# Kernel tuning notes

Hardware: AMD Instinct MI355X
Metric: run time of the kernel (lower is better)

The kernel has to match this reference:

```python
import jax, jax.numpy as jnp
from jax import lax
import numpy as np

DIM = 768        # d_model (mamba-130m)
D_IN = 1024      # vision encoder feature dim
NQ = 384         # num_queries
NB = 12          # num_blocks
BATCH = 2
LSEQ = 1024      # image tokens
DI = 2 * DIM     # mamba d_inner (expand=2)
DS = 16          # d_state
DC = 4           # d_conv
DTR = 48         # dt_rank = ceil(768/16)
NH = 16          # attention heads
HD = DIM // NH
NM = NB + 2      # mamba instances: fwd-enc, bwd-enc, one per block


def _ln(x, g, b):
    m = jnp.mean(x, -1, keepdims=True)
    v = jnp.mean((x - m) ** 2, -1, keepdims=True)
    return (x - m) * lax.rsqrt(v + 1e-5) * g + b


def _mamba(x, in_w, conv_w, conv_b, xproj_w, dt_w, dt_b, A_log, Dp, out_w):
    # x: (B, L, DIM)
    Bb = x.shape[0]
    xz = x @ in_w.T                      # (B, L, 2*DI)
    xi, z = jnp.split(xz, 2, -1)
    # depthwise causal conv1d over time
    xc = lax.conv_general_dilated(xi.transpose(0, 2, 1), conv_w[:, None, :], (1,),
                                  [(DC - 1, 0)], feature_group_count=DI,
                                  dimension_numbers=('NCH', 'OIH', 'NCH'))
    xc = jax.nn.silu((xc + conv_b[None, :, None]).transpose(0, 2, 1))  # (B, L, DI)
    dbl = xc @ xproj_w.T                 # (B, L, DTR + 2*DS)
    dt, Bm, Cm = jnp.split(dbl, [DTR, DTR + DS], -1)
    dt = jax.nn.softplus(dt @ dt_w.T + dt_b)   # (B, L, DI)
    A = -jnp.exp(A_log)                        # (DI, DS)
    dA = jnp.exp(dt[..., None] * A)            # (B, L, DI, DS)
    dBx = dt[..., None] * Bm[:, :, None, :] * xc[..., None]

    def step(h, inp):
        dA_t, dBx_t, C_t = inp
        h = dA_t * h + dBx_t
        return h, jnp.einsum('bds,bs->bd', h, C_t)

    h0 = jnp.zeros((Bb, DI, DS), x.dtype)
    _, ys = lax.scan(step, h0, (dA.transpose(1, 0, 2, 3), dBx.transpose(1, 0, 2, 3), Cm.transpose(1, 0, 2)))
    y = ys.transpose(1, 0, 2) + Dp * xc
    y = y * jax.nn.silu(z)
    return y @ out_w.T


def _local_allowed(nq, nk):
    # matches Attention.get_local_mask: query i attends to its contiguous key block
    kpq, extra = nk // nq, nk % nq
    i = jnp.arange(nq)
    start = i * kpq + jnp.minimum(i, extra)
    end = start + kpq + (i < extra)
    k = jnp.arange(nk)
    return (k[None, :] >= start[:, None]) & (k[None, :] < end[:, None])


def _mha(q_in, kv, in_w, in_b, out_w, out_b, allowed):
    # nn.MultiheadAttention(dim, 16, batch_first=True) cross-attention
    wq, wk, wv = jnp.split(in_w, 3, 0)
    bq, bk, bv = jnp.split(in_b, 3, 0)
    Bb = q_in.shape[0]
    q = (q_in @ wq.T + bq).reshape(Bb, -1, NH, HD)
    k = (kv @ wk.T + bk).reshape(Bb, -1, NH, HD)
    v = (kv @ wv.T + bv).reshape(Bb, -1, NH, HD)
    s = jnp.einsum('bqhd,bkhd->bhqk', q, k) / np.float32(np.sqrt(HD))
    s = jnp.where(allowed[None, None], s, -jnp.inf)
    a = jax.nn.softmax(s, -1)
    o = jnp.einsum('bhqk,bkhd->bqhd', a, v).reshape(Bb, -1, DIM)
    return o @ out_w.T + out_b


def _model(img_emb, queries, vision_proj_w, vision_proj_b, ln_vision_g, ln_vision_b,
           mamba_in_w, mamba_conv_w, mamba_conv_b, mamba_xproj_w, mamba_dt_w, mamba_dt_b,
           mamba_A_log, mamba_D, mamba_out_w, seq_norm_g, seq_norm_b,
           attn_in_w, attn_in_b, attn_out_w, attn_out_b, cross_w, cross_b):
    mp = lambda i: (mamba_in_w[i], mamba_conv_w[i], mamba_conv_b[i], mamba_xproj_w[i],
                    mamba_dt_w[i], mamba_dt_b[i], mamba_A_log[i], mamba_D[i], mamba_out_w[i])
    feats = _ln(img_emb @ vision_proj_w.T + vision_proj_b, ln_vision_g, ln_vision_b)
    fwd = _mamba(feats, *mp(0))
    bwd = jnp.flip(_mamba(jnp.flip(feats, 1), *mp(1)), 1)
    c = fwd + bwd + feats
    x = jnp.broadcast_to(queries, (img_emb.shape[0], NQ, DIM))
    allowed = _local_allowed(NQ, c.shape[1])
    for l in range(NB):
        x = _ln(x, seq_norm_g[l], seq_norm_b[l])
        x = _mamba(x, *mp(l + 2)) + x
        score = _mha(x, c, attn_in_w[l], attn_in_b[l], attn_out_w[l], attn_out_b[l], allowed)
        x = jnp.concatenate([x, score], -1) @ cross_w[l].T + cross_b[l]
    return x


_model_jit = jax.jit(_model)


def setup_inputs() -> dict:
    key = jax.random.key(0)
    ks = iter(jax.random.split(key, 24))
    rn = lambda shape, s=0.02: jax.random.normal(next(ks), shape, jnp.float32) * s
    A_log = jnp.broadcast_to(jnp.log(jnp.arange(1, DS + 1, dtype=jnp.float32)), (NM, DI, DS))
    return {
        'img_emb': rn((BATCH, LSEQ, D_IN), 1.0),
        'queries': rn((1, NQ, DIM)),
        'vision_proj_w': rn((DIM, D_IN)),
        'vision_proj_b': jnp.zeros((DIM,), jnp.float32),
        'ln_vision_g': jnp.ones((DIM,), jnp.float32),
        'ln_vision_b': jnp.zeros((DIM,), jnp.float32),
        'mamba_in_w': rn((NM, 2 * DI, DIM)),
        'mamba_conv_w': rn((NM, DI, DC), 0.1),
        'mamba_conv_b': jnp.zeros((NM, DI), jnp.float32),
        'mamba_xproj_w': rn((NM, DTR + 2 * DS, DI)),
        'mamba_dt_w': rn((NM, DI, DTR), 0.1),
        'mamba_dt_b': rn((NM, DI), 0.5),
        'mamba_A_log': A_log,
        'mamba_D': jnp.ones((NM, DI), jnp.float32),
        'mamba_out_w': rn((NM, DIM, DI)),
        'seq_norm_g': jnp.ones((NB, DIM), jnp.float32),
        'seq_norm_b': jnp.zeros((NB, DIM), jnp.float32),
        'attn_in_w': rn((NB, 3 * DIM, DIM)),
        'attn_in_b': jnp.zeros((NB, 3 * DIM), jnp.float32),
        'attn_out_w': rn((NB, DIM, DIM)),
        'attn_out_b': jnp.zeros((NB, DIM), jnp.float32),
        'cross_w': rn((NB, DIM, 2 * DIM)),
        'cross_b': jnp.zeros((NB, DIM), jnp.float32),
    }


def reference(img_emb, queries, vision_proj_w, vision_proj_b, ln_vision_g, ln_vision_b,
              mamba_in_w, mamba_conv_w, mamba_conv_b, mamba_xproj_w, mamba_dt_w, mamba_dt_b,
              mamba_A_log, mamba_D, mamba_out_w, seq_norm_g, seq_norm_b,
              attn_in_w, attn_in_b, attn_out_w, attn_out_b, cross_w, cross_b):
    return _model_jit(img_emb, queries, vision_proj_w, vision_proj_b, ln_vision_g, ln_vision_b,
                      mamba_in_w, mamba_conv_w, mamba_conv_b, mamba_xproj_w, mamba_dt_w, mamba_dt_b,
                      mamba_A_log, mamba_D, mamba_out_w, seq_norm_g, seq_norm_b,
                      attn_in_w, attn_in_b, attn_out_w, attn_out_b, cross_w, cross_b)
```

## Files before the change

kernel.cpp:

```cpp
#include <hip/hip_runtime.h>
#include <hip/hip_bf16.h>

#define DIMQ 768
#define D_IN 1024
#define NQ 384
#define NBK 12
#define BATCH 2
#define LSEQ 1024
#define DI 1536
#define DS 16
#define DTR 48
#define NH 16
#define HD 48

typedef __attribute__((ext_vector_type(8))) short short8;
typedef __attribute__((ext_vector_type(4))) float f32x4;

#define GF_BIAS 1
#define GF_SOFTPLUS 2
#define EPI_BIAS 1
#define EPI_ADDT 2

#define LOG2E 1.4426950408889634f

__device__ __forceinline__ unsigned short f2bf(float f) {
    unsigned int u = __builtin_bit_cast(unsigned int, f);
    u = (u + 0x7FFFu + ((u >> 16) & 1u)) >> 16;
    return (unsigned short)u;
}
__device__ __forceinline__ float bf2f(unsigned short h) {
    unsigned int u = ((unsigned int)h) << 16;
    return __builtin_bit_cast(float, u);
}

__device__ __forceinline__ void gload_lds16(const void* g, void* l) {
    __builtin_amdgcn_global_load_lds(
        (const __attribute__((address_space(1))) void*)g,
        (__attribute__((address_space(3))) void*)l, 16, 0, 0);
}

struct WTab {
    const float* src[10];
    long long dstOff[10];
    long long ps[10];
    int cum[10];
    int rows[10], cols[10], dcols[10];
    int n;
    int total;
};

__global__ void wconv_kernel(unsigned short* __restrict__ dst, WTab T)
{
    const int i = blockIdx.x * 256 + threadIdx.x;
    if (i >= T.total) return;
    int sI = 0;
    while (i >= T.cum[sI]) ++sI;
    const int e = i - (sI ? T.cum[sI - 1] : 0);
    const int dcols = T.dcols[sI];
    const int r = e / dcols;
    const int c = e - r * dcols;
    float v = 0.f;
    if (r < T.rows[sI] && c < T.cols[sI]) v = T.src[sI][(long long)r * T.cols[sI] + c];
    const unsigned short h = f2bf(v);
    const unsigned short l = f2bf(v - bf2f(h));
    dst[T.dstOff[sI] + e] = h;
    dst[T.dstOff[sI] + T.ps[sI] + e] = l;
}

__global__ __launch_bounds__(256, 4)
void gemm_direct(const float* __restrict__ Ag, const unsigned short* __restrict__ Bhl,
                 float* __restrict__ Cg, const float* __restrict__ biasg,
                 int M, int N, int K, int lda, int ldb, int ldc,
                 long long sA, long long sB, long long sC, long long sBias,
                 long long planeB, int flags)
{
    __shared__ __align__(16) unsigned short As[2][64][40];
    __shared__ __align__(16) unsigned short Bs[2][128][32];

    const int z = blockIdx.z;
    const float* A = Ag + (size_t)z * sA;
    const unsigned short* Bhi = Bhl + (size_t)z * sB;
    const unsigned short* Blo = Bhi + planeB;
    float* C = Cg + (size_t)z * sC;

    const int mBase = blockIdx.x * 64;
    const int nBase = blockIdx.y * 128;
    const int tid = threadIdx.x, lane = tid & 63, wave = tid >> 6;
    const int lm = lane & 15, lq = lane >> 4;
    const int wn = wave * 32;
    const int arow = tid >> 2, aq = tid & 3;
    const int brow = lane >> 2;
    const int bcol = (lane & 3) * 8;

    f32x4 acc[4][2] = {};
    const int ktiles = (K + 31) >> 5;

    for (int t = 0; t < ktiles; ++t) {
        const int kb = t * 32;
#pragma unroll
        for (int cc = 0; cc < 4; ++cc) {
            const int chunk = wave * 4 + cc;
            const int pl = chunk >> 3;
            const int r16 = chunk & 7;
            const unsigned short* bp = pl ? Blo : Bhi;
            const int n = nBase + r16 * 16 + brow;
            const unsigned short* g = bp + (size_t)n * ldb + kb + bcol;
            gload_lds16(g, &Bs[pl][r16 * 16][0]);
        }
        {
            const int gr = mBase + arow;
            const int col = kb + aq * 8;
            const float* src = A + (size_t)gr * lda + col;
            float v[8];
#pragma unroll
            for (int u = 0; u < 2; ++u) {
                float4 t4 = make_float4(0.f, 0.f, 0.f, 0.f);
                if (col + u * 4 < K) t4 = *(const float4*)(src + u * 4);
                v[u*4+0]=t4.x; v[u*4+1]=t4.y; v[u*4+2]=t4.z; v[u*4+3]=t4.w;
            }
            short8 ph, plv;
#pragma unroll
            for (int j = 0; j < 8; ++j) {
                unsigned short h = f2bf(v[j]);
                ph[j] = (short)h;
                plv[j] = (short)f2bf(v[j] - bf2f(h));
            }
            *(short8*)&As[0][arow][aq * 8] = ph;
            *(short8*)&As[1][arow][aq * 8] = plv;
        }
        __syncthreads();
        short8 ah[4], al[4], bh[2], bl[2];
#pragma unroll
        for (int i = 0; i < 4; ++i) {
            ah[i] = *(const short8*)&As[0][16*i + lm][lq * 8];
            al[i] = *(const short8*)&As[1][16*i + lm][lq * 8];
        }
#pragma unroll
        for (int j = 0; j < 2; ++j) {
            bh[j] = *(const short8*)&Bs[0][wn + 16*j + lm][lq * 8];
            bl[j] = *(const short8*)&Bs[1][wn + 16*j + lm][lq * 8];
        }
#pragma unroll
        for (int i = 0; i < 4; ++i)
#pragma unroll
            for (int j = 0; j < 2; ++j) {
                acc[i][j] = __builtin_amdgcn_mfma_f32_16x16x32_bf16(ah[i], bh[j], acc[i][j], 0, 0, 0);
                acc[i][j] = __builtin_amdgcn_mfma_f32_16x16x32_bf16(ah[i], bl[j], acc[i][j], 0, 0, 0);
                acc[i][j] = __builtin_amdgcn_mfma_f32_16x16x32_bf16(al[i], bh[j], acc[i][j], 0, 0, 0);
            }
        __syncthreads();
    }

#pragma unroll
    for (int i = 0; i < 4; ++i)
#pragma unroll
        for (int j = 0; j < 2; ++j)
#pragma unroll
            for (int r = 0; r < 4; ++r) {
                const int m = mBase + i*16 + lq*4 + r;
                const int n = nBase + wn + j*16 + lm;
                float v = acc[i][j][r];
                if (flags & GF_BIAS)     v += biasg[(size_t)z * sBias + n];
                if (flags & GF_SOFTPLUS) v = (v > 20.f) ? v : log1pf(expf(v));
                C[(size_t)m * ldc + n] = v;
            }
}

__global__ __launch_bounds__(256, 4)
void gemm_splitk(const float* __restrict__ Ag, const unsigned short* __restrict__ Bhl,
                 float* __restrict__ Cp,
                 int M, int kLen, int S, int lda, int ldb, int ldP,
                 long long sA, long long sB, long long planeB)
{
    __shared__ __align__(16) unsigned short As[2][64][40];
    __shared__ __align__(16) unsigned short Bs[2][128][32];

    const int bz = blockIdx.z;
    const int s = bz % S, z = bz / S;
    const int kOff = s * kLen;
    const float* A = Ag + (size_t)z * sA;
    const unsigned short* Bhi = Bhl + (size_t)z * sB;
    const unsigned short* Blo = Bhi + planeB;

    const int mBase = blockIdx.x * 64;
    const int nBase = blockIdx.y * 128;
    const int tid = threadIdx.x, lane = tid & 63, wave = tid >> 6;
    const int lm = lane & 15, lq = lane >> 4;
    const int wn = wave * 32;
    const int arow = tid >> 2, aq = tid & 3;
    const int brow = lane >> 2;
    const int bcol = (lane & 3) * 8;

    f32x4 acc[4][2] = {};
    const int ktiles = kLen >> 5;

    for (int t = 0; t < ktiles; ++t) {
        const int kb = kOff + t * 32;
#pragma unroll
        for (int cc = 0; cc < 4; ++cc) {
            const int chunk = wave * 4 + cc;
            const int pl = chunk >> 3;
            const int r16 = chunk & 7;
            const unsigned short* bp = pl ? Blo : Bhi;
            const int n = nBase + r16 * 16 + brow;
            gload_lds16(bp + (size_t)n * ldb + kb + bcol, &Bs[pl][r16 * 16][0]);
        }
        {
            const int gr = mBase + arow;
            const float* src = A + (size_t)gr * lda + kb + aq * 8;
            float v[8];
#pragma unroll
            for (int u = 0; u < 2; ++u) {
                const float4 t4 = *(const float4*)(src + u * 4);
                v[u*4+0]=t4.x; v[u*4+1]=t4.y; v[u*4+2]=t4.z; v[u*4+3]=t4.w;
            }
            short8 ph, plv;
#pragma unroll
            for (int j = 0; j < 8; ++j) {
                unsigned short h = f2bf(v[j]);
                ph[j] = (short)h;
                plv[j] = (short)f2bf(v[j] - bf2f(h));
            }
            *(short8*)&As[0][arow][aq * 8] = ph;
            *(short8*)&As[1][arow][aq * 8] = plv;
        }
        __syncthreads();
        short8 ah[4], al[4], bh[2], bl[2];
#pragma unroll
        for (int i = 0; i < 4; ++i) {
            ah[i] = *(const short8*)&As[0][16*i + lm][lq * 8];
            al[i] = *(const short8*)&As[1][16*i + lm][lq * 8];
        }
#pragma unroll
        for (int j = 0; j < 2; ++j) {
            bh[j] = *(const short8*)&Bs[0][wn + 16*j + lm][lq * 8];
            bl[j] = *(const short8*)&Bs[1][wn + 16*j + lm][lq * 8];
        }
#pragma unroll
        for (int i = 0; i < 4; ++i)
#pragma unroll
            for (int j = 0; j < 2; ++j) {
                acc[i][j] = __builtin_amdgcn_mfma_f32_16x16x32_bf16(ah[i], bh[j], acc[i][j], 0, 0, 0);
                acc[i][j] = __builtin_amdgcn_mfma_f32_16x16x32_bf16(ah[i], bl[j], acc[i][j], 0, 0, 0);
                acc[i][j] = __builtin_amdgcn_mfma_f32_16x16x32_bf16(al[i], bh[j], acc[i][j], 0, 0, 0);
            }
        __syncthreads();
    }

    float* Cb = Cp + (size_t)bz * M * ldP;
#pragma unroll
    for (int i = 0; i < 4; ++i)
#pragma unroll
        for (int j = 0; j < 2; ++j)
#pragma unroll
            for (int r = 0; r < 4; ++r) {
                const int m = mBase + i*16 + lq*4 + r;
                const int n = nBase + wn + j*16 + lm;
                Cb[(size_t)m * ldP + n] = acc[i][j][r];
            }
}

__global__ void epi_kernel(const float* __restrict__ Cp, float* __restrict__ outF,
                           const float* __restrict__ bias, const float* __restrict__ addT,
                           int Z, int S, int M, int N, int ldP, int ldOut,
                           long long sOutZ, long long sBiasZ, int ldAdd, int flags)
{
    const int n4 = N >> 2;
    const int idx = blockIdx.x * 256 + threadIdx.x;
    if (idx >= Z * M * n4) return;
    const int c4 = idx % n4;
    const int rem = idx / n4;
    const int m = rem % M;
    const int z = rem / M;
    const int n = c4 * 4;
    const float* base = Cp + ((size_t)z * S * M + m) * ldP + n;
    float4 v = *(const float4*)base;
    for (int s = 1; s < S; ++s) {
        const float4 u = *(const float4*)(base + (size_t)s * M * ldP);
        v.x += u.x; v.y += u.y; v.z += u.z; v.w += u.w;
    }
    if (flags & EPI_BIAS) {
        const float4 b4 = *(const float4*)(bias + (size_t)z * sBiasZ + n);
        v.x += b4.x; v.y += b4.y; v.z += b4.z; v.w += b4.w;
    }
    if (flags & EPI_ADDT) {
        const float4 a4 = *(const float4*)(addT + (size_t)m * ldAdd + n);
        v.x += a4.x; v.y += a4.y; v.z += a4.z; v.w += a4.w;
    }
    *(float4*)(outF + (size_t)z * sOutZ + (size_t)m * ldOut + n) = v;
}

__global__ void ln_kernel(const float* __restrict__ in, float* __restrict__ out,
                          const float* __restrict__ g, const float* __restrict__ b, int rows)
{
    const int row = blockIdx.x * 4 + (threadIdx.x >> 6);
    const int lane = threadIdx.x & 63;
    if (row >= rows) return;
    const float* p = in + (size_t)row * DIMQ;
    float v[12], s = 0.f, s2 = 0.f;
#pragma unroll
    for (int j = 0; j < 12; ++j) {
        v[j] = p[j*64 + lane];
        s += v[j];
        s2 += v[j]*v[j];
    }
#pragma unroll
    for (int o = 32; o; o >>= 1) { s += __shfl_xor(s, o); s2 += __shfl_xor(s2, o); }
    const float mean = s * (1.f/768.f);
    const float var  = s2 * (1.f/768.f) - mean*mean;
    const float inv  = rsqrtf(var + 1e-5f);
    float* q = out + (size_t)row * DIMQ;
#pragma unroll
    for (int j = 0; j < 12; ++j) {
        const int c = j*64 + lane;
        q[c] = (v[j] - mean) * inv * g[c] + b[c];
    }
}

__global__ void conv_kernel(const float* __restrict__ xz, float* __restrict__ xc,
                            const float* __restrict__ cw, const float* __restrict__ cb,
                            int Bn, int L, int instShift)
{
    const int idx = blockIdx.x * 256 + threadIdx.x;
    const int total = Bn * L * (DI/4);
    if (idx >= total) return;
    const int d4 = idx % (DI/4);
    const int t  = (idx / (DI/4)) % L;
    const int b  = idx / (L * (DI/4));
    const int inst = b >> instShift;
    const int d = d4 * 4;
    const float* base = xz + (size_t)(b * L) * 3072 + d;
    const float4 w0 = *(const float4*)(cw + (size_t)(inst*DI + d + 0) * 4);
    const float4 w1 = *(const float4*)(cw + (size_t)(inst*DI + d + 1) * 4);
    const float4 w2 = *(const float4*)(cw + (size_t)(inst*DI + d + 2) * 4);
    const float4 w3 = *(const float4*)(cw + (size_t)(inst*DI + d + 3) * 4);
    float4 acc = *(const float4*)(cb + (size_t)inst*DI + d);
    float4 xv[4];
#pragma unroll
    for (int j = 0; j < 4; ++j) {
        const int tt = t - 3 + j;
        xv[j] = (tt >= 0) ? *(const float4*)(base + (size_t)tt * 3072) : make_float4(0,0,0,0);
    }
    acc.x += xv[0].x*w0.x + xv[1].x*w0.y + xv[2].x*w0.z + xv[3].x*w0.w;
    acc.y += xv[0].y*w1.x + xv[1].y*w1.y + xv[2].y*w1.z + xv[3].y*w1.w;
    acc.z += xv[0].z*w2.x + xv[1].z*w2.y + xv[2].z*w2.z + xv[3].z*w2.w;
    acc.w += xv[0].w*w3.x + xv[1].w*w3.y + xv[2].w*w3.z + xv[3].w*w3.w;
    float4 o;
    o.x = acc.x / (1.f + expf(-acc.x));
    o.y = acc.y / (1.f + expf(-acc.y));
    o.z = acc.z / (1.f + expf(-acc.z));
    o.w = acc.w / (1.f + expf(-acc.w));
    *(float4*)(xc + (size_t)(b * L + t) * DI + d) = o;
}

__global__ __launch_bounds__(256)
void scan_p1(const float* __restrict__ dt, const float* __restrict__ dbl,
             const float* __restrict__ xc, const float* __restrict__ A_log,
             float* __restrict__ hend, float* __restrict__ sumdt,
             int L, int CL, int Bn, int instShift)
{
    const int d = blockIdx.x * 256 + threadIdx.x;
    const int b = blockIdx.y;
    const int c = blockIdx.z;
    const int inst = b >> instShift;
    const float* ap = A_log + ((size_t)inst * DI + d) * DS;
    float A2[16];
#pragma unroll
    for (int s = 0; s < 16; ++s) A2[s] = -expf(ap[s]) * LOG2E;
    float h[16] = {};
    float sd = 0.f;
    const int t0 = c * CL;
    const size_t rowbase = (size_t)b * L;
    for (int t = t0; t < t0 + CL; ++t) {
        const size_t row = rowbase + t;
        const float dtv = dt[row * DI + d];
        const float xcv = xc[row * DI + d];
        float Bv[16];
        *(float4*)(Bv + 0)  = *(const float4*)(dbl + row * 80 + 48);
        *(float4*)(Bv + 4)  = *(const float4*)(dbl + row * 80 + 52);
        *(float4*)(Bv + 8)  = *(const float4*)(dbl + row * 80 + 56);
        *(float4*)(Bv + 12) = *(const float4*)(dbl + row * 80 + 60);
        sd += dtv;
        const float bx = dtv * xcv;
#pragma unroll
        for (int s = 0; s < 16; ++s)
            h[s] = exp2f(dtv * A2[s]) * h[s] + bx * Bv[s];
    }
    float* hp = hend + (((size_t)c * Bn + b) * DI + d) * DS;
#pragma unroll
    for (int s = 0; s < 16; s += 4)
        *(float4*)(hp + s) = make_float4(h[s], h[s+1], h[s+2], h[s+3]);
    sumdt[((size_t)c * Bn + b) * DI + d] = sd;
}

__global__ void scan_p2(const float* __restrict__ hend, const float* __restrict__ sumdt,
                        const float* __restrict__ A_log, float* __restrict__ hstart,
                        int NC, int Bn, int instShift)
{
    const int gid = blockIdx.x * 256 + threadIdx.x;
    const int s = gid & 15;
    const int rem = gid >> 4;
    const int d = rem % DI;
    const int b = rem / DI;
    const int inst = b >> instShift;
    const float A2 = -expf(A_log[((size_t)inst * DI + d) * DS + s]) * LOG2E;
    float carry = 0.f;
    for (int c = 0; c < NC; ++c) {
        const size_t off = (((size_t)c * Bn + b) * DI + d) * DS + s;
        hstart[off] = carry;
        carry = exp2f(A2 * sumdt[((size_t)c * Bn + b) * DI + d]) * carry + hend[off];
    }
}

__global__ __launch_bounds__(256)
void scan_p3(const float* __restrict__ dt, const float* __restrict__ dbl,
             const float* __restrict__ xc, const float* __restrict__ xz,
             const float* __restrict__ A_log, const float* __restrict__ Dp,
             const float* __restrict__ hstart, float* __restrict__ y,
             int L, int CL, int Bn, int instShift)
{
    const int d = blockIdx.x * 256 + threadIdx.x;
    const int b = blockIdx.y;
    const int c = blockIdx.z;
    const int inst = b >> instShift;
    const float* ap = A_log + ((size_t)inst * DI + d) * DS;
    float A2[16];
#pragma unroll
    for (int s = 0; s < 16; ++s) A2[s] = -expf(ap[s]) * LOG2E;
    const float Dd = Dp[(size_t)inst * DI + d];
    float h[16];
    const float* hp = hstart + (((size_t)c * Bn + b) * DI + d) * DS;
#pragma unroll
    for (int s = 0; s < 16; s += 4) {
        const float4 t4 = *(const float4*)(hp + s);
        h[s] = t4.x; h[s+1] = t4.y; h[s+2] = t4.z; h[s+3] = t4.w;
    }
    const int t0 = c * CL;
    const size_t rowbase = (size_t)b * L;
    for (int t = t0; t < t0 + CL; ++t) {
        const size_t row = rowbase + t;
        const float dtv = dt[row * DI + d];
        const float xcv = xc[row * DI + d];
        const float zv  = xz[row * 3072 + DI + d];
        float Bv[16], Cv[16];
        *(float4*)(Bv + 0)  = *(const float4*)(dbl + row * 80 + 48);
        *(float4*)(Bv + 4)  = *(const float4*)(dbl + row * 80 + 52);
        *(float4*)(Bv + 8)  = *(const float4*)(dbl + row * 80 + 56);
        *(float4*)(Bv + 12) = *(const float4*)(dbl + row * 80 + 60);
        *(float4*)(Cv + 0)  = *(const float4*)(dbl + row * 80 + 64);
        *(float4*)(Cv + 4)  = *(const float4*)(dbl + row * 80 + 68);
        *(float4*)(Cv + 8)  = *(const float4*)(dbl + row * 80 + 72);
        *(float4*)(Cv + 12) = *(const float4*)(dbl + row * 80 + 76);
        const float bx = dtv * xcv;
#pragma unroll
        for (int s = 0; s < 16; ++s)
            h[s] = exp2f(dtv * A2[s]) * h[s] + bx * Bv[s];
        float p0 = 0.f, p1 = 0.f, p2 = 0.f, p3 = 0.f;
#pragma unroll
        for (int s = 0; s < 4; ++s) {
            p0 += h[s]      * Cv[s];
            p1 += h[s + 4]  * Cv[s + 4];
            p2 += h[s + 8]  * Cv[s + 8];
            p3 += h[s + 12] * Cv[s + 12];
        }
        const float p = (p0 + p1) + (p2 + p3);
        y[row * DI + d] = (p + Dd * xcv) * (zv / (1.f + expf(-zv)));
    }
}

__global__ void attn_kernel(const float* __restrict__ q, const float* __restrict__ kv,
                            float* __restrict__ o)
{
    const int bi = blockIdx.x;
    const int b = bi / NQ, i = bi % NQ;
    const int tid = threadIdx.x;
    const int h = tid >> 2, r = tid & 3;
    int start, len;
    if (i < 256) { start = 3*i; len = 3; } else { start = 2*i + 256; len = 2; }
    const float* qp = q + (size_t)bi * DIMQ + h*48 + r*12;
    float qv[12];
#pragma unroll
    for (int u = 0; u < 12; ++u) qv[u] = qp[u];
    float s[3] = {-1e30f, -1e30f, -1e30f};
    for (int j = 0; j < len; ++j) {
        const float* kp = kv + (size_t)(b*LSEQ + start + j) * 1536 + h*48 + r*12;
        float p = 0.f;
#pragma unroll
        for (int u = 0; u < 12; ++u) p += qv[u] * kp[u];
        p += __shfl_xor(p, 1);
        p += __shfl_xor(p, 2);
        s[j] = p * 0.14433756729740644f;
    }
    const float mx = fmaxf(s[0], fmaxf(s[1], s[2]));
    float e[3];
    e[0] = expf(s[0]-mx); e[1] = expf(s[1]-mx); e[2] = expf(s[2]-mx);
    const float inv = 1.f / (e[0] + e[1] + e[2]);
    float ov[12] = {};
    for (int j = 0; j < len; ++j) {
        const float w = e[j] * inv;
        const float* vp = kv + (size_t)(b*LSEQ + start + j) * 1536 + 768 + h*48 + r*12;
#pragma unroll
        for (int u = 0; u < 12; ++u) ov[u] += w * vp[u];
    }
    float* op = o + (size_t)bi * DIMQ + h*48 + r*12;
#pragma unroll
    for (int u = 0; u < 12; ++u) op[u] = ov[u];
}

__global__ void flip_kernel(float* __restrict__ X2)
{
    const int idx = blockIdx.x * 256 + threadIdx.x;
    if (idx >= 2*1024*192) return;
    const int d4 = idx % 192;
    const int t  = (idx / 192) % 1024;
    const int b  = idx / (192 * 1024);
    const size_t dst = ((size_t)((2+b)*1024 + t)) * DIMQ + d4*4;
    const size_t src = ((size_t)(b*1024 + (1023 - t))) * DIMQ + d4*4;
    *(float4*)(X2 + dst) = *(const float4*)(X2 + src);
}

__global__ void combine_kernel(const float* __restrict__ oe, const float* __restrict__ feats,
                               float* __restrict__ c)
{
    const int idx = blockIdx.x * 256 + threadIdx.x;
    if (idx >= 2*1024*192) return;
    const int d4 = idx % 192;
    const int t  = (idx / 192) % 1024;
    const int b  = idx / (192 * 1024);
    const size_t fw = ((size_t)(b*1024 + t)) * DIMQ + d4*4;
    const size_t bw = ((size_t)((2+b)*1024 + (1023 - t))) * DIMQ + d4*4;
    const float4 a = *(const float4*)(oe + fw);
    const float4 bb = *(const float4*)(oe + bw);
    const float4 f = *(const float4*)(feats + fw);
    float4 o;
    o.x = a.x + bb.x + f.x; o.y = a.y + bb.y + f.y;
    o.z = a.z + bb.z + f.z; o.w = a.w + bb.w + f.w;
    *(float4*)(c + fw) = o;
}

__global__ void qinit_kernel(float* __restrict__ x, const float* __restrict__ queries)
{
    const int idx = blockIdx.x * 256 + threadIdx.x;
    if (idx >= 2*NQ*192) return;
    const int d4 = idx % 192;
    const int i  = (idx / 192) % NQ;
    *(float4*)(x + (size_t)idx * 4) = *(const float4*)(queries + ((size_t)i * DIMQ + d4*4));
}

extern "C" void kernel_launch(void* const* d_in, const int* in_sizes, int n_in,
                              void* d_out, int out_size, void* d_ws, size_t ws_size,
                              hipStream_t stream) {
    const float* img_emb  = (const float*)d_in[0];
    const float* queries  = (const float*)d_in[1];
    const float* vis_w    = (const float*)d_in[2];
    const float* vis_b    = (const float*)d_in[3];
    const float* lnv_g    = (const float*)d_in[4];
    const float* lnv_b    = (const float*)d_in[5];
    const float* m_in_w   = (const float*)d_in[6];
    const float* m_conv_w = (const float*)d_in[7];
    const float* m_conv_b = (const float*)d_in[8];
    const float* m_xp_w   = (const float*)d_in[9];
    const float* m_dt_w   = (const float*)d_in[10];
    const float* m_dt_b   = (const float*)d_in[11];
    const float* m_A_log  = (const float*)d_in[12];
    const float* m_D      = (const float*)d_in[13];
    const float* m_out_w  = (const float*)d_in[14];
    const float* sn_g     = (const float*)d_in[15];
    const float* sn_b     = (const float*)d_in[16];
    const float* a_in_w   = (const float*)d_in[17];
    const float* a_in_b   = (const float*)d_in[18];
    const float* a_out_w  = (const float*)d_in[19];
    const float* a_out_b  = (const float*)d_in[20];
    const float* cr_w     = (const float*)d_in[21];
    const float* cr_b     = (const float*)d_in[22];
    float* out = (float*)d_out;

    float* ws = (float*)d_ws;
    float* X2   = ws; ws += (size_t)4096*768;
    float* xzb  = ws; ws += (size_t)4096*3072;
    float* xcb  = ws; ws += (size_t)4096*1536;
    float* dblb = ws; ws += (size_t)4096*80;
    float* dtb  = ws; ws += (size_t)4096*1536;
    float* yb   = ws; ws += (size_t)4096*1536;
    float* oe   = ws; ws += (size_t)4096*768;
    float* cbuf = ws; ws += (size_t)2048*768;
    float* xbuf = ws; ws += (size_t)768*768;
    float* xn   = ws; ws += (size_t)768*768;
    float* x1s  = ws; ws += (size_t)768*1536;
    float* qb   = ws; ws += (size_t)768*768;
    float* ob   = ws; ws += (size_t)768*768;
    float* Cp   = ws; ws += (size_t)2359296;
    unsigned short* wenc = (unsigned short*)ws; ws += (size_t)16908288/2;
    unsigned short* wlay = (unsigned short*)ws; ws += (size_t)14745600/2;

    const long long P_VIS = 768LL*1024;
    const long long P_IN  = 3072LL*768;
    const long long P_XP  = 128LL*1536;
    const long long P_DT  = 1536LL*64;
    const long long P_OUT = 768LL*1536;
    const long long P_AIN = 2304LL*768;
    const long long P_AOUT= 768LL*768;
    const long long P_CR  = 768LL*1536;
    const long long off_vis   = 0;
    const long long off_encIn = 2*P_VIS;
    const long long off_encXp = off_encIn + 4*P_IN;
    const long long off_encDt = off_encXp + 4*P_XP;
    const long long off_encOut= off_encDt + 4*P_DT;
    const long long off_in  = 0;
    const long long off_xp  = 2*P_IN;
    const long long off_dt  = off_xp + 2*P_XP;
    const long long off_out = off_dt + 2*P_DT;
    const long long off_aIn = off_out + 2*P_OUT;
    const long long off_aOut= off_aIn + 2*P_AIN;
    const long long off_cr  = off_aOut + 2*P_AOUT;

    auto addSeg = [](WTab& T, const float* src, int rows, int cols, int drows, int dcols,
                     long long dstOff) {
        const int k = T.n;
        T.src[k] = src; T.rows[k] = rows; T.cols[k] = cols; T.dcols[k] = dcols;
        T.ps[k] = (long long)drows * dcols;
        T.dstOff[k] = dstOff;
        T.total += drows * dcols;
        T.cum[k] = T.total;
        T.n = k + 1;
    };

    auto GD = [&](const float* A, const unsigned short* Bhl, long long planeB,
                  float* C, const float* bias,
                  int M, int N, int K, int lda, int ldb, int ldc,
                  long long sA, long long sB, long long sC, long long sBias,
                  int Z, int flags) {
        dim3 grid(M/64, N/128, Z);
        gemm_direct<<<grid, 256, 0, stream>>>(A, Bhl, C, bias, M, N, K, lda, ldb, ldc,
                                              sA, sB, sC, sBias, planeB, flags);
    };
    auto GS = [&](const float* A, const unsigned short* Bhl, long long planeB,
                  int M, int Ntile, int kLen, int S, int lda, int ldb, int ldP,
                  long long sA, long long sB, int Z) {
        dim3 grid(M/64, Ntile/128, Z*S);
        gemm_splitk<<<grid, 256, 0, stream>>>(A, Bhl, Cp, M, kLen, S, lda, ldb, ldP,
                                              sA, sB, planeB);
    };
    auto EPI = [&](float* outF, const float* bias, const float* addT,
                   int Z, int S, int M, int N, int ldP, int ldOut,
                   long long sOutZ, long long sBiasZ, int ldAdd, int flags) {
        const int total = Z * M * (N/4);
        epi_kernel<<<(total+255)/256, 256, 0, stream>>>(Cp, outF, bias, addT, Z, S, M, N,
                                                        ldP, ldOut, sOutZ, sBiasZ, ldAdd, flags);
    };

    {
        WTab T = {}; T.n = 0; T.total = 0;
        addSeg(T, vis_w, 768, 1024, 768, 1024, off_vis);
        addSeg(T, m_in_w,               3072, 768, 3072, 768, off_encIn);
        addSeg(T, m_in_w + 3072*768,    3072, 768, 3072, 768, off_encIn + 2*P_IN);
        addSeg(T, m_xp_w,               80, 1536, 128, 1536, off_encXp);
        addSeg(T, m_xp_w + 80*1536,     80, 1536, 128, 1536, off_encXp + 2*P_XP);
        addSeg(T, m_dt_w,               1536, 48, 1536, 64, off_encDt);
        addSeg(T, m_dt_w + 1536*48,     1536, 48, 1536, 64, off_encDt + 2*P_DT);
        addSeg(T, m_out_w,              768, 1536, 768, 1536, off_encOut);
        addSeg(T, m_out_w + 768*1536,   768, 1536, 768, 1536, off_encOut + 2*P_OUT);
        wconv_kernel<<<(T.total+255)/256, 256, 0, stream>>>(wenc, T);
    }

    GD(img_emb, wenc + off_vis, P_VIS, oe, vis_b,
       2048, 768, 1024, 1024, 1024, 768, 0,0,0,0, 1, GF_BIAS);
    ln_kernel<<<512, 256, 0, stream>>>(oe, X2, lnv_g, lnv_b, 2048);
    flip_kernel<<<(2*1024*192 + 255)/256, 256, 0, stream>>>(X2);
    qinit_kernel<<<(2*NQ*192 + 255)/256, 256, 0, stream>>>(xbuf, queries);

    GD(X2, wenc + off_encIn, P_IN, xzb, nullptr,
       2048, 3072, 768, 768, 768, 3072, 2048LL*768, 2*P_IN, 2048LL*3072, 0, 2, 0);
    conv_kernel<<<(4*1024*384 + 255)/256, 256, 0, stream>>>(xzb, xcb, m_conv_w, m_conv_b, 4, 1024, 1);
    GS(xcb, wenc + off_encXp, P_XP, 2048, 128, 384, 4, 1536, 1536, 128,
       2048LL*1536, 2*P_XP, 2);
    EPI(dblb, nullptr, nullptr, 2, 4, 2048, 80, 128, 80, 2048LL*80, 0, 0, 0);
    GD(dblb, wenc + off_encDt, P_DT, dtb, m_dt_b,
       2048, 1536, 48, 80, 64, 1536, 2048LL*80, 2*P_DT, 2048LL*1536, 1536, 2,
       GF_BIAS | GF_SOFTPLUS);
    {
        const int NC = 8, CL = 128;
        float* hend   = oe;
        float* hstart = oe + (size_t)NC*4*DI*DS;
        float* sumdt  = oe + (size_t)2*NC*4*DI*DS;
        scan_p1<<<dim3(6, 4, NC), 256, 0, stream>>>(dtb, dblb, xcb, m_A_log, hend, sumdt, 1024, CL, 4, 1);
        scan_p2<<<(4*DI*DS)/256, 256, 0, stream>>>(hend, sumdt, m_A_log, hstart, NC, 4, 1);
        scan_p3<<<dim3(6, 4, NC), 256, 0, stream>>>(dtb, dblb, xcb, xzb, m_A_log, m_D, hstart, yb, 1024, CL, 4, 1);
    }
    GD(yb, wenc + off_encOut, P_OUT, oe, nullptr,
       2048, 768, 1536, 1536, 1536, 768, 2048LL*1536, 2*P_OUT, 2048LL*768, 0, 2, 0);
    combine_kernel<<<(2*1024*192 + 255)/256, 256, 0, stream>>>(oe, X2, cbuf);

    for (int l = 0; l < NBK; ++l) {
        const int li = l + 2;
        {
            WTab T = {}; T.n = 0; T.total = 0;
            addSeg(T, m_in_w + (size_t)li*3072*768, 3072, 768, 3072, 768, off_in);
            addSeg(T, m_xp_w + (size_t)li*80*1536,  80, 1536, 128, 1536, off_xp);
            addSeg(T, m_dt_w + (size_t)li*1536*48,  1536, 48, 1536, 64, off_dt);
            addSeg(T, m_out_w + (size_t)li*768*1536, 768, 1536, 768, 1536, off_out);
            addSeg(T, a_in_w + (size_t)l*2304*768,  2304, 768, 2304, 768, off_aIn);
            addSeg(T, a_out_w + (size_t)l*768*768,  768, 768, 768, 768, off_aOut);
            addSeg(T, cr_w + (size_t)l*768*1536,    768, 1536, 768, 1536, off_cr);
            wconv_kernel<<<(T.total+255)/256, 256, 0, stream>>>(wlay, T);
        }
        ln_kernel<<<192, 256, 0, stream>>>(xbuf, xn, sn_g + (size_t)l*768, sn_b + (size_t)l*768, 768);
        GD(xn, wlay + off_in, P_IN, xzb, nullptr,
           768, 3072, 768, 768, 768, 3072, 0,0,0,0, 1, 0);
        conv_kernel<<<(2*NQ*384 + 255)/256, 256, 0, stream>>>(
            xzb, xcb, m_conv_w + (size_t)li*DI*4, m_conv_b + (size_t)li*DI, 2, NQ, 8);
        GS(xcb, wlay + off_xp, P_XP, 768, 128, 96, 16, 1536, 1536, 128, 0, 0, 1);
        EPI(dblb, nullptr, nullptr, 1, 16, 768, 80, 128, 80, 0, 0, 0, 0);
        GD(dblb, wlay + off_dt, P_DT, dtb, m_dt_b + (size_t)li*1536,
           768, 1536, 48, 80, 64, 1536, 0,0,0,0, 1, GF_BIAS | GF_SOFTPLUS);
        {
            const int NC = 12, CL = 32;
            const float* Ap = m_A_log + (size_t)li*DI*DS;
            float* hend   = oe;
            float* hstart = oe + (size_t)NC*2*DI*DS;
            float* sumdt  = oe + (size_t)2*NC*2*DI*DS;
            scan_p1<<<dim3(6, 2, NC), 256, 0, stream>>>(dtb, dblb, xcb, Ap, hend, sumdt, NQ, CL, 2, 8);
            scan_p2<<<(2*DI*DS)/256, 256, 0, stream>>>(hend, sumdt, Ap, hstart, NC, 2, 8);
            scan_p3<<<dim3(6, 2, NC), 256, 0, stream>>>(dtb, dblb, xcb, xzb, Ap, m_D + (size_t)li*DI,
                                                        hstart, yb, NQ, CL, 2, 8);
        }
        GS(yb, wlay + off_out, P_OUT, 768, 768, 384, 4, 1536, 1536, 768, 0, 0, 1);
        EPI(x1s, nullptr, xn, 1, 4, 768, 768, 768, 1536, 0, 0, 768, EPI_ADDT);
        GS(x1s, wlay + off_aIn, P_AIN, 768, 768, 192, 4, 1536, 768, 768, 0, 0, 1);
        EPI(qb, a_in_b + (size_t)l*2304, nullptr, 1, 4, 768, 768, 768, 768, 0, 0, 0, EPI_BIAS);
        GD(cbuf, wlay + off_aIn + 768LL*768, P_AIN, oe, a_in_b + (size_t)l*2304 + 768,
           2048, 1536, 768, 768, 768, 1536, 0,0,0,0, 1, GF_BIAS);
        attn_kernel<<<2*NQ, 64, 0, stream>>>(qb, oe, ob);
        GS(ob, wlay + off_aOut, P_AOUT, 768, 768, 192, 4, 768, 768, 768, 0, 0, 1);
        EPI(x1s + 768, a_out_b + (size_t)l*768, nullptr, 1, 4, 768, 768, 768, 1536, 0, 0, 0, EPI_BIAS);
        float* dst = (l == NBK - 1) ? out : xbuf;
        GS(x1s, wlay + off_cr, P_CR, 768, 768, 384, 4, 1536, 1536, 768, 0, 0, 1);
        EPI(dst, cr_b + (size_t)l*768, nullptr, 1, 4, 768, 768, 768, 768, 0, 0, 0, EPI_BIAS);
    }
}
```

Measured before the change: 4.638 ms.

## Double-buffer LDS tiles in split-bf16 GEMM kernels to overlap loads with MFMA

Both GEMM kernels now keep two LDS stages for the A and B tiles. The next tile's B async loads and A global reads are issued before the current tile's MFMAs, and the converted A tile is written to the other buffer afterwards, so one barrier per k-step is dropped. The aim is to hide global memory latency behind the matrix compute. In exchange the kernels use twice the LDS and the launch-bounds occupancy hint drops from 4 to 3 blocks per CU.

After: 4.504 ms. 1.03x faster.

```diff
diff --git a/kernel.cpp b/kernel.cpp
--- a/kernel.cpp
+++ b/kernel.cpp
@@ -67,15 +67,15 @@
     dst[T.dstOff[sI] + T.ps[sI] + e] = l;
 }
 
-__global__ __launch_bounds__(256, 4)
+__global__ __launch_bounds__(256, 3)
 void gemm_direct(const float* __restrict__ Ag, const unsigned short* __restrict__ Bhl,
                  float* __restrict__ Cg, const float* __restrict__ biasg,
                  int M, int N, int K, int lda, int ldb, int ldc,
                  long long sA, long long sB, long long sC, long long sBias,
                  long long planeB, int flags)
 {
-    __shared__ __align__(16) unsigned short As[2][64][40];
-    __shared__ __align__(16) unsigned short Bs[2][128][32];
+    __shared__ __align__(16) unsigned short As[2][2][64][40];
+    __shared__ __align__(16) unsigned short Bs[2][2][128][32];
 
     const int z = blockIdx.z;
     const float* A = Ag + (size_t)z * sA;
@@ -92,11 +92,9 @@
     const int brow = lane >> 2;
     const int bcol = (lane & 3) * 8;
 
-    f32x4 acc[4][2] = {};
     const int ktiles = (K + 31) >> 5;
 
-    for (int t = 0; t < ktiles; ++t) {
-        const int kb = t * 32;
+    auto issueB = [&](int t, int buf) {
 #pragma unroll
         for (int cc = 0; cc < 4; ++cc) {
             const int chunk = wave * 4 + cc;
@@ -104,41 +102,52 @@
             const int r16 = chunk & 7;
             const unsigned short* bp = pl ? Blo : Bhi;
             const int n = nBase + r16 * 16 + brow;
-            const unsigned short* g = bp + (size_t)n * ldb + kb + bcol;
-            gload_lds16(g, &Bs[pl][r16 * 16][0]);
-        }
-        {
-            const int gr = mBase + arow;
-            const int col = kb + aq * 8;
-            const float* src = A + (size_t)gr * lda + col;
-            float v[8];
-#pragma unroll
-            for (int u = 0; u < 2; ++u) {
-                float4 t4 = make_float4(0.f, 0.f, 0.f, 0.f);
-                if (col + u * 4 < K) t4 = *(const float4*)(src + u * 4);
-                v[u*4+0]=t4.x; v[u*4+1]=t4.y; v[u*4+2]=t4.z; v[u*4+3]=t4.w;
-            }
-            short8 ph, plv;
-#pragma unroll
-            for (int j = 0; j < 8; ++j) {
-                unsigned short h = f2bf(v[j]);
-                ph[j] = (short)h;
-                plv[j] = (short)f2bf(v[j] - bf2f(h));
-            }
-            *(short8*)&As[0][arow][aq * 8] = ph;
-            *(short8*)&As[1][arow][aq * 8] = plv;
-        }
+            gload_lds16(bp + (size_t)n * ldb + t * 32 + bcol, &Bs[buf][pl][r16 * 16][0]);
+        }
+    };
+    auto loadA = [&](int t, float* v) {
+        const int col = t * 32 + aq * 8;
+        const float* src = A + (size_t)(mBase + arow) * lda + col;
+#pragma unroll
+        for (int u = 0; u < 2; ++u) {
+            float4 t4 = make_float4(0.f, 0.f, 0.f, 0.f);
+            if (col + u * 4 < K) t4 = *(const float4*)(src + u * 4);
+            v[u*4+0]=t4.x; v[u*4+1]=t4.y; v[u*4+2]=t4.z; v[u*4+3]=t4.w;
+        }
+    };
+    auto writeA = [&](const float* v, int buf) {
+        short8 ph, plv;
+#pragma unroll
+        for (int j = 0; j < 8; ++j) {
+            unsigned short h = f2bf(v[j]);
+            ph[j] = (short)h;
+            plv[j] = (short)f2bf(v[j] - bf2f(h));
+        }
+        *(short8*)&As[buf][0][arow][aq * 8] = ph;
+        *(short8*)&As[buf][1][arow][aq * 8] = plv;
+    };
+
+    float av[8];
+    issueB(0, 0);
+    loadA(0, av);
+    writeA(av, 0);
+
+    f32x4 acc[4][2] = {};
+    for (int t = 0; t < ktiles; ++t) {
+        const int buf = t & 1;
         __syncthreads();
+        const bool more = (t + 1) < ktiles;
+        if (more) { issueB(t + 1, buf ^ 1); loadA(t + 1, av); }
         short8 ah[4], al[4], bh[2], bl[2];
 #pragma unroll
         for (int i = 0; i < 4; ++i) {
-            ah[i] = *(const short8*)&As[0][16*i + lm][lq * 8];
-            al[i] = *(const short8*)&As[1][16*i + lm][lq * 8];
+            ah[i] = *(const short8*)&As[buf][0][16*i + lm][lq * 8];
+            al[i] = *(const short8*)&As[buf][1][16*i + lm][lq * 8];
         }
 #pragma unroll
         for (int j = 0; j < 2; ++j) {
-            bh[j] = *(const short8*)&Bs[0][wn + 16*j + lm][lq * 8];
-            bl[j] = *(const short8*)&Bs[1][wn + 16*j + lm][lq * 8];
+            bh[j] = *(const short8*)&Bs[buf][0][wn + 16*j + lm][lq * 8];
+            bl[j] = *(const short8*)&Bs[buf][1][wn + 16*j + lm][lq * 8];
         }
 #pragma unroll
         for (int i = 0; i < 4; ++i)
@@ -148,7 +157,7 @@
                 acc[i][j] = __builtin_amdgcn_mfma_f32_16x16x32_bf16(ah[i], bl[j], acc[i][j], 0, 0, 0);
                 acc[i][j] = __builtin_amdgcn_mfma_f32_16x16x32_bf16(al[i], bh[j], acc[i][j], 0, 0, 0);
             }
-        __syncthreads();
+        if (more) writeA(av, buf ^ 1);
     }
 
 #pragma unroll
@@ -166,14 +175,14 @@
             }
 }
 
-__global__ __launch_bounds__(256, 4)
+__global__ __launch_bounds__(256, 3)
 void gemm_splitk(const float* __restrict__ Ag, const unsigned short* __restrict__ Bhl,
                  float* __restrict__ Cp,
                  int M, int kLen, int S, int lda, int ldb, int ldP,
                  long long sA, long long sB, long long planeB)
 {
-    __shared__ __align__(16) unsigned short As[2][64][40];
-    __shared__ __align__(16) unsigned short Bs[2][128][32];
+    __shared__ __align__(16) unsigned short As[2][2][64][40];
+    __shared__ __align__(16) unsigned short Bs[2][2][128][32];
 
     const int bz = blockIdx.z;
     const int s = bz % S, z = bz / S;
@@ -191,11 +200,9 @@
     const int brow = lane >> 2;
     const int bcol = (lane & 3) * 8;
 
-    f32x4 acc[4][2] = {};
     const int ktiles = kLen >> 5;
 
-    for (int t = 0; t < ktiles; ++t) {
-        const int kb = kOff + t * 32;
+    auto issueB = [&](int t, int buf) {
 #pragma unroll
         for (int cc = 0; cc < 4; ++cc) {
             const int chunk = wave * 4 + cc;
@@ -203,38 +210,50 @@
             const int r16 = chunk & 7;
             const unsigned short* bp = pl ? Blo : Bhi;
             const int n = nBase + r16 * 16 + brow;
-            gload_lds16(bp + (size_t)n * ldb + kb + bcol, &Bs[pl][r16 * 16][0]);
-        }
-        {
-            const int gr = mBase + arow;
-            const float* src = A + (size_t)gr * lda + kb + aq * 8;
-            float v[8];
-#pragma unroll
-            for (int u = 0; u < 2; ++u) {
-                const float4 t4 = *(const float4*)(src + u * 4);
-                v[u*4+0]=t4.x; v[u*4+1]=t4.y; v[u*4+2]=t4.z; v[u*4+3]=t4.w;
-            }
-            short8 ph, plv;
-#pragma unroll
-            for (int j = 0; j < 8; ++j) {
-                unsigned short h = f2bf(v[j]);
-                ph[j] = (short)h;
-                plv[j] = (short)f2bf(v[j] - bf2f(h));
-            }
-            *(short8*)&As[0][arow][aq * 8] = ph;
-            *(short8*)&As[1][arow][aq * 8] = plv;
-        }
+            gload_lds16(bp + (size_t)n * ldb + kOff + t * 32 + bcol, &Bs[buf][pl][r16 * 16][0]);
+        }
+    };
+    auto loadA = [&](int t, float* v) {
+        const float* src = A + (size_t)(mBase + arow) * lda + kOff + t * 32 + aq * 8;
+#pragma unroll
+        for (int u = 0; u < 2; ++u) {
+            const float4 t4 = *(const float4*)(src + u * 4);
+            v[u*4+0]=t4.x; v[u*4+1]=t4.y; v[u*4+2]=t4.z; v[u*4+3]=t4.w;
+        }
+    };
+    auto writeA = [&](const float* v, int buf) {
+        short8 ph, plv;
+#pragma unroll
+        for (int j = 0; j < 8; ++j) {
+            unsigned short h = f2bf(v[j]);
+            ph[j] = (short)h;
+            plv[j] = (short)f2bf(v[j] - bf2f(h));
+        }
+        *(short8*)&As[buf][0][arow][aq * 8] = ph;
+        *(short8*)&As[buf][1][arow][aq * 8] = plv;
+    };
+
+    float av[8];
+    issueB(0, 0);
+    loadA(0, av);
+    writeA(av, 0);
+
+    f32x4 acc[4][2] = {};
+    for (int t = 0; t < ktiles; ++t) {
+        const int buf = t & 1;
         __syncthreads();
+        const bool more = (t + 1) < ktiles;
+        if (more) { issueB(t + 1, buf ^ 1); loadA(t + 1, av); }
         short8 ah[4], al[4], bh[2], bl[2];
 #pragma unroll
         for (int i = 0; i < 4; ++i) {
-            ah[i] = *(const short8*)&As[0][16*i + lm][lq * 8];
-            al[i] = *(const short8*)&As[1][16*i + lm][lq * 8];
+            ah[i] = *(const short8*)&As[buf][0][16*i + lm][lq * 8];
+            al[i] = *(const short8*)&As[buf][1][16*i + lm][lq * 8];
         }
 #pragma unroll
         for (int j = 0; j < 2; ++j) {
-            bh[j] = *(const short8*)&Bs[0][wn + 16*j + lm][lq * 8];
-            bl[j] = *(const short8*)&Bs[1][wn + 16*j + lm][lq * 8];
+            bh[j] = *(const short8*)&Bs[buf][0][wn + 16*j + lm][lq * 8];
+            bl[j] = *(const short8*)&Bs[buf][1][wn + 16*j + lm][lq * 8];
         }
 #pragma unroll
         for (int i = 0; i < 4; ++i)
@@ -244,7 +263,7 @@
                 acc[i][j] = __builtin_amdgcn_mfma_f32_16x16x32_bf16(ah[i], bl[j], acc[i][j], 0, 0, 0);
                 acc[i][j] = __builtin_amdgcn_mfma_f32_16x16x32_bf16(al[i], bh[j], acc[i][j], 0, 0, 0);
             }
-        __syncthreads();
+        if (more) writeA(av, buf ^ 1);
     }
 
     float* Cb = Cp + (size_t)bz * M * ldP;
```
